# Performance work log

Hardware: AMD Instinct MI355X
Metric: run time of the kernel (lower is better)

## Reference

```python
import jax, jax.numpy as jnp
import numpy as np
from jax import lax

B, C, H, W = 16, 512, 32, 32
CQ = C // 8  # 64
EPS = 1e-5
NEG_SLOPE = 0.2


def _conv1x1(x, Wm, b):
    # x: [B,C,H,W], Wm: [O,C] (1x1 conv kernel squeezed), b: [O]
    return jnp.einsum('oc,bchw->bohw', Wm, x) + b[None, :, None, None]


def _calc_mean_std(feat):
    b, c = feat.shape[:2]
    v = feat.reshape(b, c, -1)
    mean = v.mean(axis=2)[:, :, None, None]
    var = v.var(axis=2, ddof=1) + EPS  # torch .var is unbiased
    std = jnp.sqrt(var)[:, :, None, None]
    return mean, std


def setup_inputs() -> dict:
    key = jax.random.key(0)
    ks = jax.random.split(key, 8)
    s = 0.02
    return {
        'inp': jax.random.normal(ks[0], (B, C, H, W), jnp.float32),
        'x': jax.random.normal(ks[1], (B, C, H, W), jnp.float32),
        'y': jax.random.normal(ks[2], (B, C, H, W), jnp.float32),
        'Wq': jax.random.normal(ks[3], (CQ, C), jnp.float32) * s,
        'bq': jnp.zeros((CQ,), jnp.float32),
        'Wk': jax.random.normal(ks[4], (CQ, C), jnp.float32) * s,
        'bk': jnp.zeros((CQ,), jnp.float32),
        'Wv': jax.random.normal(ks[5], (C, C), jnp.float32) * s,
        'bv': jnp.zeros((C,), jnp.float32),
        'Wc': jax.random.normal(ks[6], (C, 2 * C, 3, 3), jnp.float32) * s,
        'bc': jnp.zeros((C,), jnp.float32),
        'alpha': jnp.ones((1,), jnp.float32),
        'beta': jnp.ones((1,), jnp.float32),
    }


def reference(inp, x, y, Wq, bq, Wk, bk, Wv, bv, Wc, bc, alpha, beta):
    b, c, h, w = x.shape
    n = h * w
    t = float(CQ) ** 0.5  # default temperature sqrt(c_in//8)

    # --- identity-row attention: query from x, key from y ---
    pq = _conv1x1(x, Wq, bq).reshape(b, CQ, n)   # [b,cq,n]
    pk = _conv1x1(y, Wk, bk).reshape(b, CQ, n)
    pv = _conv1x1(x, Wv, bv).reshape(b, c, n)    # [b,c,n]
    attn_iden = jax.nn.softmax(jnp.einsum('bcn,bcm->bnm', pq, pk) / t, axis=-1)

    # --- pose-row attention: query from y, key from x ---
    pq_p = _conv1x1(y, Wq, bq).reshape(b, CQ, n)
    pk_p = _conv1x1(x, Wk, bk).reshape(b, CQ, n)
    attn_pose = jax.nn.softmax(jnp.einsum('bcn,bcm->bnm', pq_p, pk_p) / t, axis=-1)

    # x_update = bmm(value, attn_iden^T): out[c,m] = sum_n pv[c,n]*attn[m,n]
    x_update = jnp.einsum('bcn,bmn->bcm', pv, attn_iden).reshape(b, c, h, w)
    x_update = (1.0 - beta) * x + beta * x_update

    # --- AdaIN: normalize inp, re-affine with x stats ---
    t_mean, t_std = _calc_mean_std(x)
    i_mean, i_std = _calc_mean_std(inp)
    adained = (inp - i_mean) / i_std * t_std + t_mean

    # reverse attention combine with (1 - attn_pose)
    rev = jnp.einsum('bcn,bmn->bcm', adained.reshape(b, c, n), 1.0 - attn_pose)
    rev = rev.reshape(b, c, h, w)
    rev = (1.0 - alpha) * rev + alpha * adained

    # --- conv_comp: 3x3 conv (2C -> C), same padding, LeakyReLU(0.2) ---
    cat = jnp.concatenate([x_update, rev], axis=1)  # [b,2c,h,w]
    out = lax.conv_general_dilated(
        cat, Wc, window_strides=(1, 1), padding='SAME',
        dimension_numbers=('NCHW', 'OIHW', 'NCHW'))
    out = out + bc[None, :, None, None]
    out = jnp.where(out >= 0, out, NEG_SLOPE * out)
    return out
```

## Files before the change

kernel.cpp:

```cpp
#include <hip/hip_runtime.h>

typedef unsigned short u16;
typedef unsigned int u32;

using bf16x8 = __attribute__((ext_vector_type(8))) __bf16;
using f32x4  = __attribute__((ext_vector_type(4))) float;
using u16x4  = __attribute__((ext_vector_type(4))) unsigned short;

__device__ __forceinline__ f32x4 MFMA(bf16x8 a, bf16x8 b, f32x4 c) {
    return __builtin_amdgcn_mfma_f32_16x16x32_bf16(a, b, c, 0, 0, 0);
}

__device__ __forceinline__ u16 f2bf(float f) {
    u32 u = __builtin_bit_cast(u32, f);
    u = (u + 0x7FFFu + ((u >> 16) & 1u)) >> 16;
    return (u16)u;
}
__device__ __forceinline__ float bf2f(u16 h) {
    return __builtin_bit_cast(float, (u32)h << 16);
}

typedef const __attribute__((address_space(1))) unsigned int* gp_t;
typedef __attribute__((address_space(3))) unsigned int* lp_t;

__device__ __forceinline__ void gload16(const void* g, void* l) {
    __builtin_amdgcn_global_load_lds((gp_t)g, (lp_t)l, 16, 0, 0);
}

#define NPADR  1156

static constexpr size_t OFF_XT   = 0;
static constexpr size_t OFF_YT   = OFF_XT  + (size_t)16*1024*512*2;
static constexpr size_t OFF_PJX  = OFF_YT  + (size_t)16*1024*512*2;
static constexpr size_t OFF_PJY  = OFF_PJX + (size_t)16*1024*128*2;
static constexpr size_t OFF_PV   = OFF_PJY + (size_t)16*1024*128*2;
static constexpr size_t OFF_AD   = OFF_PV  + (size_t)16*512*1024*2;
static constexpr size_t OFF_ATTN = OFF_AD  + (size_t)16*512*1024*2;
static constexpr size_t OFF_ATT2 = OFF_ATTN+ (size_t)16*1024*1024*2;
static constexpr size_t OFF_CATT = OFF_ATT2+ (size_t)16*1024*1024*2;
static constexpr size_t OFF_WQK  = OFF_CATT+ (size_t)16*1156*1024*2;
static constexpr size_t OFF_WV   = OFF_WQK + (size_t)128*512*2;
static constexpr size_t OFF_WT   = OFF_WV  + (size_t)512*512*2;
static constexpr size_t OFF_SA   = OFF_WT  + (size_t)9*512*1024*2;
static constexpr size_t OFF_OA   = OFF_SA  + (size_t)16*512*4;
static constexpr size_t OFF_TM   = OFF_OA  + (size_t)16*512*4;

__global__ __launch_bounds__(256) void k_prep_w(const float* __restrict__ Wq,
                                                const float* __restrict__ Wk,
                                                const float* __restrict__ Wv,
                                                u16* __restrict__ wqk, u16* __restrict__ wv) {
    int i = blockIdx.x * 256 + threadIdx.x;
    if (i < 128 * 512) {
        float v = (i < 64 * 512) ? Wq[i] : Wk[i - 64 * 512];
        wqk[i] = f2bf(v);
    }
    if (i < 512 * 512) wv[i] = f2bf(Wv[i]);
}

__global__ __launch_bounds__(256) void k_prep_wt(const float* __restrict__ Wc, u16* __restrict__ wt) {
    int e = blockIdx.x * 256 + threadIdx.x;
    const float* src = Wc + (size_t)e * 9;
#pragma unroll
    for (int tap = 0; tap < 9; tap++) wt[(size_t)tap * 524288 + e] = f2bf(src[tap]);
}

__global__ __launch_bounds__(256) void k_border(u16* __restrict__ catT) {
    int cell = blockIdx.x, b = blockIdx.y;
    int row, col;
    if (cell < 34)       { row = 0;  col = cell; }
    else if (cell < 68)  { row = 33; col = cell - 34; }
    else if (cell < 100) { row = cell - 68 + 1;  col = 0; }
    else                 { row = cell - 100 + 1; col = 33; }
    u16* dst = catT + ((size_t)b * NPADR + row * 34 + col) * 1024;
    u16x4 z = {0, 0, 0, 0};
    ((u16x4*)dst)[threadIdx.x] = z;
}

__global__ __launch_bounds__(256) void k_stats(const float* __restrict__ x, const float* __restrict__ inp,
                                               u16* __restrict__ ad, float* __restrict__ tmA) {
    int row = blockIdx.x;
    int t = threadIdx.x;
    const float4* xr = (const float4*)(x + (size_t)row * 1024);
    const float4* ir = (const float4*)(inp + (size_t)row * 1024);
    float4 a = xr[t], c = ir[t];
    float s1 = a.x + a.y + a.z + a.w;
    float s2 = a.x * a.x + a.y * a.y + a.z * a.z + a.w * a.w;
    float p1 = c.x + c.y + c.z + c.w;
    float p2 = c.x * c.x + c.y * c.y + c.z * c.z + c.w * c.w;
#pragma unroll
    for (int m = 32; m; m >>= 1) {
        s1 += __shfl_xor(s1, m); s2 += __shfl_xor(s2, m);
        p1 += __shfl_xor(p1, m); p2 += __shfl_xor(p2, m);
    }
    __shared__ float red[4][4];
    __shared__ float bcast[2];
    int wv = t >> 6;
    if ((t & 63) == 0) { red[wv][0] = s1; red[wv][1] = s2; red[wv][2] = p1; red[wv][3] = p2; }
    __syncthreads();
    if (t == 0) {
        s1 = red[0][0] + red[1][0] + red[2][0] + red[3][0];
        s2 = red[0][1] + red[1][1] + red[2][1] + red[3][1];
        p1 = red[0][2] + red[1][2] + red[2][2] + red[3][2];
        p2 = red[0][3] + red[1][3] + red[2][3] + red[3][3];
        float tm = s1 * (1.0f / 1024.0f);
        float ts = sqrtf((s2 - 1024.0f * tm * tm) * (1.0f / 1023.0f) + 1e-5f);
        float im = p1 * (1.0f / 1024.0f);
        float is = sqrtf((p2 - 1024.0f * im * im) * (1.0f / 1023.0f) + 1e-5f);
        float sc = ts / is;
        bcast[0] = sc; bcast[1] = tm - im * sc;
        tmA[row] = tm;
    }
    __syncthreads();
    float sc = bcast[0], of = bcast[1];
    u16x4 r;
    r[0] = f2bf(c.x * sc + of); r[1] = f2bf(c.y * sc + of);
    r[2] = f2bf(c.z * sc + of); r[3] = f2bf(c.w * sc + of);
    ((u16x4*)(ad + (size_t)row * 1024))[t] = r;
}

__global__ __launch_bounds__(256) void k_transpose(const float* __restrict__ x, const float* __restrict__ y,
                                                   u16* __restrict__ xT, u16* __restrict__ yT) {
    __shared__ float tile[64][65];
    int b = blockIdx.y;
    int ct = blockIdx.x >> 4;
    int nt = blockIdx.x & 15;
    const float* src = blockIdx.z ? y : x;
    u16* dst = blockIdx.z ? yT : xT;
    int c0 = ct * 64, n0 = nt * 64;
    int ln = threadIdx.x & 63, wv = threadIdx.x >> 6;
#pragma unroll
    for (int i = 0; i < 16; i++) {
        int cl = wv + i * 4;
        tile[cl][ln] = src[((size_t)(b * 512 + c0 + cl)) * 1024 + n0 + ln];
    }
    __syncthreads();
#pragma unroll
    for (int i = 0; i < 16; i++) {
        int nl = wv + i * 4;
        dst[((size_t)(b * 1024 + n0 + nl)) * 512 + c0 + ln] = f2bf(tile[ln][nl]);
    }
}

template <int KTOT, int LDA, int LDB>
__device__ __forceinline__ void gemm128(const u16* __restrict__ Aorig, const u16* __restrict__ Borig,
                                        f32x4 (&acc)[4][4]) {
    __shared__ __align__(16) u16 lds[32768];
    constexpr int NT = KTOT / 32;
    const int tid = threadIdx.x;
    const int l = tid & 63, w = tid >> 6;
    const int lr = l & 15, lg = l >> 4;
    const int moff = (w >> 1) * 64, coff = (w & 1) * 64;
    char* ldsb = (char*)lds;
    auto stage = [&](const u16* orig, int ldx, int bufByte) {
#pragma unroll
        for (int it = 0; it < 2; it++) {
            int slot = it * 256 + tid;
            gload16(orig + (size_t)(slot & 127) * ldx + (slot >> 7) * 8,
                    ldsb + bufByte + it * 4096 + w * 1024);
        }
    };
    auto stageT = [&](int t, int s) {
        stage(Aorig + t * 32, LDA, s * 8192);
        stage(Borig + t * 32, LDB, 32768 + s * 8192);
    };
    stageT(0, 0);
    stageT(1, 1);
    stageT(2, 2);
#pragma unroll 1
    for (int q = 0; q < NT; q++) {
        int qq = q + 3; if (qq >= NT) qq -= NT;
        stageT(qq, (q + 3) & 3);
        asm volatile("s_waitcnt vmcnt(12)" ::: "memory");
        __builtin_amdgcn_s_barrier();
        const char* A = ldsb + (q & 3) * 8192;
        const char* B = ldsb + 32768 + (q & 3) * 8192;
        bf16x8 af[4], bb[4];
#pragma unroll
        for (int i = 0; i < 4; i++) af[i] = *(const bf16x8*)(A + lg * 2048 + (moff + 16 * i + lr) * 16);
#pragma unroll
        for (int i = 0; i < 4; i++) bb[i] = *(const bf16x8*)(B + lg * 2048 + (coff + 16 * i + lr) * 16);
        __builtin_amdgcn_s_setprio(1);
#pragma unroll
        for (int ri = 0; ri < 4; ri++)
#pragma unroll
            for (int ci = 0; ci < 4; ci++) acc[ri][ci] = MFMA(af[ri], bb[ci], acc[ri][ci]);
        __builtin_amdgcn_s_setprio(0);
        __builtin_amdgcn_s_barrier();
    }
    asm volatile("s_waitcnt vmcnt(0)" ::: "memory");
}

__global__ __launch_bounds__(256) void k_proj(const u16* __restrict__ xT, const u16* __restrict__ yT,
                                              const u16* __restrict__ wqk, const float* __restrict__ bq,
                                              const float* __restrict__ bk, u16* __restrict__ pjx,
                                              u16* __restrict__ pjy) {
    int b = blockIdx.y;
    const u16* S = blockIdx.z ? yT : xT;
    u16* D = blockIdx.z ? pjy : pjx;
    int nb = blockIdx.x * 128;
    f32x4 acc[4][4];
#pragma unroll
    for (int i = 0; i < 4; i++)
#pragma unroll
        for (int j = 0; j < 4; j++) acc[i][j] = f32x4{0.f, 0.f, 0.f, 0.f};
    gemm128<512, 512, 512>(S + ((size_t)b * 1024 + nb) * 512, wqk, acc);
    int l = threadIdx.x & 63, w = threadIdx.x >> 6;
    int lr = l & 15, lg = l >> 4;
    int moff = (w >> 1) * 64, coff = (w & 1) * 64;
#pragma unroll
    for (int ri = 0; ri < 4; ri++) {
#pragma unroll
        for (int r = 0; r < 4; r++) {
            int n = nb + moff + 16 * ri + 4 * lg + r;
#pragma unroll
            for (int ci = 0; ci < 4; ci++) {
                int cq = coff + 16 * ci + lr;
                float bias = (cq < 64) ? bq[cq] : bk[cq - 64];
                D[((size_t)b * 1024 + n) * 128 + cq] = f2bf(acc[ri][ci][r] + bias);
            }
        }
    }
}

__global__ __launch_bounds__(256) void k_pv(const u16* __restrict__ xT, const u16* __restrict__ wv,
                                            const float* __restrict__ bv, u16* __restrict__ pv) {
    int b = blockIdx.z;
    int mb = blockIdx.y * 128;
    int nb = blockIdx.x * 128;
    f32x4 acc[4][4];
#pragma unroll
    for (int i = 0; i < 4; i++)
#pragma unroll
        for (int j = 0; j < 4; j++) acc[i][j] = f32x4{0.f, 0.f, 0.f, 0.f};
    gemm128<512, 512, 512>(wv + (size_t)mb * 512, xT + ((size_t)b * 1024 + nb) * 512, acc);
    int l = threadIdx.x & 63, w = threadIdx.x >> 6;
    int lr = l & 15, lg = l >> 4;
    int moff = (w >> 1) * 64, coff = (w & 1) * 64;
#pragma unroll
    for (int ri = 0; ri < 4; ri++) {
#pragma unroll
        for (int r = 0; r < 4; r++) {
            int co = mb + moff + 16 * ri + 4 * lg + r;
            float bias = bv[co];
#pragma unroll
            for (int ci = 0; ci < 4; ci++) {
                int n = nb + coff + 16 * ci + lr;
                pv[((size_t)b * 512 + co) * 1024 + n] = f2bf(acc[ri][ci][r] + bias);
            }
        }
    }
}

__global__ __launch_bounds__(256) void k_score(const u16* __restrict__ pjx, const u16* __restrict__ pjy,
                                               u16* __restrict__ attnA, u16* __restrict__ attnB) {
    const u16* qT = blockIdx.y ? pjy : pjx;
    const u16* kT = blockIdx.y ? pjx : pjy;
    u16* attn = blockIdx.y ? attnB : attnA;
    int g = blockIdx.x * 4 + (threadIdx.x >> 6);
    int b = g >> 6, rb = g & 63;
    int l = threadIdx.x & 63, lr = l & 15, lg = l >> 4;
    int mb = rb * 16;
    const u16* qbase = qT + ((size_t)b * 1024 + mb + lr) * 128 + lg * 8;
    bf16x8 a0 = *(const bf16x8*)(qbase);
    bf16x8 a1 = *(const bf16x8*)(qbase + 32);
    const u16* kbase = kT + ((size_t)b * 1024 + lr) * 128 + 64 + lg * 8;
    f32x4 zero = {0.f, 0.f, 0.f, 0.f};
    float mrun[4] = {-1e30f, -1e30f, -1e30f, -1e30f};
    float srun[4] = {0.f, 0.f, 0.f, 0.f};
    for (int cf = 0; cf < 64; cf++) {
        bf16x8 b0 = *(const bf16x8*)(kbase + (size_t)cf * 16 * 128);
        bf16x8 b1 = *(const bf16x8*)(kbase + (size_t)cf * 16 * 128 + 32);
        f32x4 acc = zero;
        acc = MFMA(a0, b0, acc);
        acc = MFMA(a1, b1, acc);
#pragma unroll
        for (int r = 0; r < 4; r++) {
            float v = acc[r] * 0.125f;
            float mn = fmaxf(mrun[r], v);
            srun[r] = srun[r] * __expf(mrun[r] - mn) + __expf(v - mn);
            mrun[r] = mn;
        }
    }
#pragma unroll
    for (int m = 1; m < 16; m <<= 1) {
#pragma unroll
        for (int r = 0; r < 4; r++) {
            float mo = __shfl_xor(mrun[r], m);
            float so = __shfl_xor(srun[r], m);
            float mn = fmaxf(mrun[r], mo);
            srun[r] = srun[r] * __expf(mrun[r] - mn) + so * __expf(mo - mn);
            mrun[r] = mn;
        }
    }
    float inv[4];
#pragma unroll
    for (int r = 0; r < 4; r++) inv[r] = 1.0f / srun[r];
    for (int cf = 0; cf < 64; cf++) {
        bf16x8 b0 = *(const bf16x8*)(kbase + (size_t)cf * 16 * 128);
        bf16x8 b1 = *(const bf16x8*)(kbase + (size_t)cf * 16 * 128 + 32);
        f32x4 acc = zero;
        acc = MFMA(a0, b0, acc);
        acc = MFMA(a1, b1, acc);
#pragma unroll
        for (int r = 0; r < 4; r++) {
            float v = __expf(acc[r] * 0.125f - mrun[r]) * inv[r];
            attn[((size_t)b * 1024 + mb + 4 * lg + r) * 1024 + cf * 16 + lr] = f2bf(v);
        }
    }
}

__global__ __launch_bounds__(256) void k_value(const u16* __restrict__ attnA, const u16* __restrict__ attnB,
                                               const u16* __restrict__ pv, const u16* __restrict__ ad,
                                               const u16* __restrict__ xT, const float* __restrict__ tmA,
                                               const float* __restrict__ alpha, const float* __restrict__ beta,
                                               u16* __restrict__ catT) {
    int z = blockIdx.z;
    int b = z & 15, var = z >> 4;
    const u16* attn = var ? attnB : attnA;
    const u16* V = var ? ad : pv;
    int mb = blockIdx.x * 128;
    int cb = blockIdx.y * 128;
    f32x4 acc[4][4];
#pragma unroll
    for (int i = 0; i < 4; i++)
#pragma unroll
        for (int j = 0; j < 4; j++) acc[i][j] = f32x4{0.f, 0.f, 0.f, 0.f};
    gemm128<1024, 1024, 1024>(attn + ((size_t)b * 1024 + mb) * 1024,
                              V + ((size_t)b * 512 + cb) * 1024, acc);
    int l = threadIdx.x & 63, w = threadIdx.x >> 6;
    int lr = l & 15, lg = l >> 4;
    int moff = (w >> 1) * 64, coff = (w & 1) * 64;
    float sc = var ? alpha[0] : beta[0];
#pragma unroll
    for (int ri = 0; ri < 4; ri++) {
#pragma unroll
        for (int r = 0; r < 4; r++) {
            int m = mb + moff + 16 * ri + 4 * lg + r;
            int pidx = ((m >> 5) + 1) * 34 + (m & 31) + 1;
#pragma unroll
            for (int ci = 0; ci < 4; ci++) {
                int c = cb + coff + 16 * ci + lr;
                float av = acc[ri][ci][r];
                float res;
                if (var == 0) {
                    float xv = bf2f(xT[((size_t)b * 1024 + m) * 512 + c]);
                    res = (1.f - sc) * xv + sc * av;
                } else {
                    float tm = tmA[b * 512 + c];
                    float adv = bf2f(ad[((size_t)b * 512 + c) * 1024 + m]);
                    res = (1.f - sc) * (1024.f * tm - av) + sc * adv;
                }
                catT[((size_t)b * NPADR + pidx) * 1024 + (var ? 512 : 0) + c] = f2bf(res);
            }
        }
    }
}

__global__ __launch_bounds__(256, 2) void k_conv(const u16* __restrict__ wt, const u16* __restrict__ catT,
                                                 const float* __restrict__ bc, float* __restrict__ out) {
    extern __shared__ __align__(16) char dyn[];
    const int tid = threadIdx.x;
    const int l = tid & 63, w = tid >> 6;
    const int lr = l & 15, lg = l >> 4;
    const int b = blockIdx.z;
    const int ob = blockIdx.x * 128;
    const int pb = blockIdx.y * 128;
    const int r0 = blockIdx.y * 4;
    const int ooff = (w >> 1) * 64, poff = (w & 1) * 64;
    const u16* catB = catT + (size_t)b * NPADR * 1024 + (size_t)r0 * 34 * 1024;

    auto stageB = [&](int ckb, int bsel) {
        char* base = dyn + 40960 + bsel * 16384;
        const u16* src0 = catB + ckb;
#pragma unroll
        for (int it = 0; it < 4; it++) {
            if (tid < 204)
                gload16(src0 + (size_t)tid * 1024 + it * 8, base + it * 4096 + w * 1024);
        }
    };
    auto stageA = [&](int tap, int ckb, int slot) {
        char* base = dyn + slot * 8192;
        const u16* src0 = wt + ((size_t)tap * 512 + ob) * 1024 + ckb;
#pragma unroll
        for (int it = 0; it < 2; it++) {
            int s = it * 256 + tid;
            gload16(src0 + (size_t)(s & 127) * 1024 + (s >> 7) * 8,
                    base + it * 4096 + w * 1024);
        }
    };

    int aoff[4], rbase[4];
#pragma unroll
    for (int i = 0; i < 4; i++) {
        aoff[i] = lg * 2048 + (ooff + 16 * i + lr) * 16;
        int p = poff + 16 * i + lr;
        rbase[i] = ((p >> 5) + 1) * 34 + (p & 31) + 1;
    }

    f32x4 acc[4][4];
#pragma unroll
    for (int i = 0; i < 4; i++)
#pragma unroll
        for (int j = 0; j < 4; j++) acc[i][j] = f32x4{0.f, 0.f, 0.f, 0.f};

    stageA(0, 0, 0);
    stageB(0, 0);
    stageA(1, 0, 1);
    stageA(2, 0, 2);
    stageA(3, 0, 3);
    int phase = 0;
#pragma unroll 1
    for (int ckI = 0; ckI < 32; ckI++) {
#pragma unroll
        for (int tap = 0; tap < 9; tap++, phase++) {
            {
                int t4 = tap + 4;
                int c4 = ckI + (t4 >= 9);
                if (t4 >= 9) t4 -= 9;
                if (c4 >= 32) c4 = 0;
                stageA(t4, c4 * 32, (phase + 4) % 5);
            }
            if (tap == 5) {
                int cn = ckI + 1;
                stageB((cn >= 32 ? 0 : cn) * 32, cn & 1);
            }
            if (tap >= 5) asm volatile("s_waitcnt vmcnt(12)" ::: "memory");
            else          asm volatile("s_waitcnt vmcnt(8)" ::: "memory");
            __builtin_amdgcn_s_barrier();
            const char* A = dyn + (phase % 5) * 8192;
            const char* B = dyn + 40960 + (ckI & 1) * 16384;
            const int drow = (tap / 3 - 1) * 34 + (tap % 3 - 1);
            bf16x8 af[4], bb[4];
#pragma unroll
            for (int i = 0; i < 4; i++) af[i] = *(const bf16x8*)(A + aoff[i]);
#pragma unroll
            for (int i = 0; i < 4; i++) bb[i] = *(const bf16x8*)(B + lg * 4096 + (rbase[i] + drow) * 16);
            __builtin_amdgcn_s_setprio(1);
#pragma unroll
            for (int ri = 0; ri < 4; ri++)
#pragma unroll
                for (int ci = 0; ci < 4; ci++) acc[ri][ci] = MFMA(af[ri], bb[ci], acc[ri][ci]);
            __builtin_amdgcn_s_setprio(0);
            __builtin_amdgcn_s_barrier();
        }
    }
    asm volatile("s_waitcnt vmcnt(0)" ::: "memory");
#pragma unroll
    for (int ri = 0; ri < 4; ri++) {
#pragma unroll
        for (int r = 0; r < 4; r++) {
            int o = ob + ooff + 16 * ri + 4 * lg + r;
            float bias = bc[o];
#pragma unroll
            for (int ci = 0; ci < 4; ci++) {
                int p = pb + poff + 16 * ci + lr;
                float v = acc[ri][ci][r] + bias;
                v = (v >= 0.f) ? v : 0.2f * v;
                out[((size_t)b * 512 + o) * 1024 + p] = v;
            }
        }
    }
}

extern "C" void kernel_launch(void* const* d_in, const int* in_sizes, int n_in,
                              void* d_out, int out_size, void* d_ws, size_t ws_size,
                              hipStream_t stream) {
    (void)in_sizes; (void)n_in; (void)out_size; (void)ws_size;
    const float* inp = (const float*)d_in[0];
    const float* x   = (const float*)d_in[1];
    const float* y   = (const float*)d_in[2];
    const float* Wq  = (const float*)d_in[3];
    const float* bq  = (const float*)d_in[4];
    const float* Wk  = (const float*)d_in[5];
    const float* bk  = (const float*)d_in[6];
    const float* Wv  = (const float*)d_in[7];
    const float* bv  = (const float*)d_in[8];
    const float* Wc  = (const float*)d_in[9];
    const float* bc  = (const float*)d_in[10];
    const float* alpha = (const float*)d_in[11];
    const float* beta  = (const float*)d_in[12];
    float* out = (float*)d_out;

    char* ws = (char*)d_ws;
    u16* xT   = (u16*)(ws + OFF_XT);
    u16* yT   = (u16*)(ws + OFF_YT);
    u16* pjx  = (u16*)(ws + OFF_PJX);
    u16* pjy  = (u16*)(ws + OFF_PJY);
    u16* pv   = (u16*)(ws + OFF_PV);
    u16* ad   = (u16*)(ws + OFF_AD);
    u16* attnA = (u16*)(ws + OFF_ATTN);
    u16* attnB = (u16*)(ws + OFF_ATT2);
    u16* catT = (u16*)(ws + OFF_CATT);
    u16* wqk  = (u16*)(ws + OFF_WQK);
    u16* wv   = (u16*)(ws + OFF_WV);
    u16* wt   = (u16*)(ws + OFF_WT);
    float* tmA = (float*)(ws + OFF_TM);

    hipFuncSetAttribute((const void*)k_conv, hipFuncAttributeMaxDynamicSharedMemorySize, 73728);

    k_prep_w<<<1024, 256, 0, stream>>>(Wq, Wk, Wv, wqk, wv);
    k_prep_wt<<<2048, 256, 0, stream>>>(Wc, wt);
    k_border<<<dim3(132, 16), 256, 0, stream>>>(catT);
    k_stats<<<8192, 256, 0, stream>>>(x, inp, ad, tmA);
    k_transpose<<<dim3(128, 16, 2), 256, 0, stream>>>(x, y, xT, yT);
    k_proj<<<dim3(8, 16, 2), 256, 0, stream>>>(xT, yT, wqk, bq, bk, pjx, pjy);
    k_pv<<<dim3(8, 4, 16), 256, 0, stream>>>(xT, wv, bv, pv);
    k_score<<<dim3(256, 2), 256, 0, stream>>>(pjx, pjy, attnA, attnB);
    k_value<<<dim3(8, 4, 32), 256, 0, stream>>>(attnA, attnB, pv, ad, xT, tmA, alpha, beta, catT);
    k_conv<<<dim3(4, 8, 16), 256, 73728, stream>>>(wt, catT, bc, out);
}
```

Baseline: 439.9 us.

## Enlarge conv tile to 256 pixels with 8-wave blocks and shallower weight pipeline

The implicit-GEMM 3x3 conv now uses 512-thread blocks covering 128 output channels by 256 pixels (8 image rows), halving the number of blocks along the pixel axis. Each weight tile staged in LDS is therefore reused by twice as many pixels, and the halo overhead per input tile drops (10 padded rows for 8 output rows instead of 6 for 4). To fit LDS, the weight ring buffer shrinks from 5 to 3 slots, so prefetch runs 2 taps ahead instead of 4. This lowers global traffic per FLOP but risks more exposed load latency and lower occupancy with 512-thread blocks.

```diff
diff --git a/kernel.cpp b/kernel.cpp
--- a/kernel.cpp
+++ b/kernel.cpp
@@ -356,7 +356,7 @@
     }
 }
 
-__global__ __launch_bounds__(256, 2) void k_conv(const u16* __restrict__ wt, const u16* __restrict__ catT,
+__global__ __launch_bounds__(512, 2) void k_conv(const u16* __restrict__ wt, const u16* __restrict__ catT,
                                                  const float* __restrict__ bc, float* __restrict__ out) {
     extern __shared__ __align__(16) char dyn[];
     const int tid = threadIdx.x;
@@ -364,36 +364,34 @@
     const int lr = l & 15, lg = l >> 4;
     const int b = blockIdx.z;
     const int ob = blockIdx.x * 128;
-    const int pb = blockIdx.y * 128;
-    const int r0 = blockIdx.y * 4;
-    const int ooff = (w >> 1) * 64, poff = (w & 1) * 64;
+    const int pb = blockIdx.y * 256;
+    const int r0 = blockIdx.y * 8;
+    const int ow = w >> 2, pw = w & 3;
     const u16* catB = catT + (size_t)b * NPADR * 1024 + (size_t)r0 * 34 * 1024;
 
-    auto stageB = [&](int ckb, int bsel) {
-        char* base = dyn + 40960 + bsel * 16384;
-        const u16* src0 = catB + ckb;
-#pragma unroll
-        for (int it = 0; it < 4; it++) {
-            if (tid < 204)
-                gload16(src0 + (size_t)tid * 1024 + it * 8, base + it * 4096 + w * 1024);
-        }
+    auto stageA = [&](int tap, int ck, int slot) {
+        char* base = dyn + slot * 8192;
+        int row = tid & 127, g = tid >> 7;
+        gload16(wt + ((size_t)tap * 512 + ob + row) * 1024 + ck + g * 8,
+                base + g * 2048 + row * 16);
     };
-    auto stageA = [&](int tap, int ckb, int slot) {
-        char* base = dyn + slot * 8192;
-        const u16* src0 = wt + ((size_t)tap * 512 + ob) * 1024 + ckb;
-#pragma unroll
-        for (int it = 0; it < 2; it++) {
-            int s = it * 256 + tid;
-            gload16(src0 + (size_t)(s & 127) * 1024 + (s >> 7) * 8,
-                    base + it * 4096 + w * 1024);
+    auto stageB = [&](int ck, int sel) {
+        char* base = dyn + 24576 + sel * 24576;
+#pragma unroll
+        for (int it = 0; it < 3; it++) {
+            int idx = it * 512 + tid;
+            int g = idx / 384;
+            int row = idx - g * 384;
+            gload16(catB + (size_t)row * 1024 + ck + g * 8,
+                    base + g * 6144 + row * 16);
         }
     };
 
     int aoff[4], rbase[4];
 #pragma unroll
     for (int i = 0; i < 4; i++) {
-        aoff[i] = lg * 2048 + (ooff + 16 * i + lr) * 16;
-        int p = poff + 16 * i + lr;
+        aoff[i] = lg * 2048 + (ow * 64 + 16 * i + lr) * 16;
+        int p = pw * 64 + 16 * i + lr;
         rbase[i] = ((p >> 5) + 1) * 34 + (p & 31) + 1;
     }
 
@@ -406,35 +404,33 @@
     stageA(0, 0, 0);
     stageB(0, 0);
     stageA(1, 0, 1);
-    stageA(2, 0, 2);
-    stageA(3, 0, 3);
     int phase = 0;
 #pragma unroll 1
     for (int ckI = 0; ckI < 32; ckI++) {
 #pragma unroll
         for (int tap = 0; tap < 9; tap++, phase++) {
             {
-                int t4 = tap + 4;
-                int c4 = ckI + (t4 >= 9);
-                if (t4 >= 9) t4 -= 9;
-                if (c4 >= 32) c4 = 0;
-                stageA(t4, c4 * 32, (phase + 4) % 5);
+                int t2 = tap + 2;
+                int c2 = ckI + (t2 >= 9);
+                if (t2 >= 9) t2 -= 9;
+                if (c2 >= 32) c2 = 0;
+                stageA(t2, c2 * 32, (phase + 2) % 3);
             }
             if (tap == 5) {
                 int cn = ckI + 1;
                 stageB((cn >= 32 ? 0 : cn) * 32, cn & 1);
             }
-            if (tap >= 5) asm volatile("s_waitcnt vmcnt(12)" ::: "memory");
-            else          asm volatile("s_waitcnt vmcnt(8)" ::: "memory");
+            if (tap >= 5 && tap <= 7) asm volatile("s_waitcnt vmcnt(5)" ::: "memory");
+            else                      asm volatile("s_waitcnt vmcnt(2)" ::: "memory");
             __builtin_amdgcn_s_barrier();
-            const char* A = dyn + (phase % 5) * 8192;
-            const char* B = dyn + 40960 + (ckI & 1) * 16384;
+            const char* A = dyn + (phase % 3) * 8192;
+            const char* B = dyn + 24576 + (ckI & 1) * 24576;
             const int drow = (tap / 3 - 1) * 34 + (tap % 3 - 1);
             bf16x8 af[4], bb[4];
 #pragma unroll
             for (int i = 0; i < 4; i++) af[i] = *(const bf16x8*)(A + aoff[i]);
 #pragma unroll
-            for (int i = 0; i < 4; i++) bb[i] = *(const bf16x8*)(B + lg * 4096 + (rbase[i] + drow) * 16);
+            for (int i = 0; i < 4; i++) bb[i] = *(const bf16x8*)(B + lg * 6144 + (rbase[i] + drow) * 16);
             __builtin_amdgcn_s_setprio(1);
 #pragma unroll
             for (int ri = 0; ri < 4; ri++)
@@ -449,11 +445,11 @@
     for (int ri = 0; ri < 4; ri++) {
 #pragma unroll
         for (int r = 0; r < 4; r++) {
-            int o = ob + ooff + 16 * ri + 4 * lg + r;
+            int o = ob + ow * 64 + 16 * ri + 4 * lg + r;
             float bias = bc[o];
 #pragma unroll
             for (int ci = 0; ci < 4; ci++) {
-                int p = pb + poff + 16 * ci + lr;
+                int p = pb + pw * 64 + 16 * ci + lr;
                 float v = acc[ri][ci][r] + bias;
                 v = (v >= 0.f) ? v : 0.2f * v;
                 out[((size_t)b * 512 + o) * 1024 + p] = v;
@@ -507,5 +503,5 @@
     k_pv<<<dim3(8, 4, 16), 256, 0, stream>>>(xT, wv, bv, pv);
     k_score<<<dim3(256, 2), 256, 0, stream>>>(pjx, pjy, attnA, attnB);
     k_value<<<dim3(8, 4, 32), 256, 0, stream>>>(attnA, attnB, pv, ad, xT, tmA, alpha, beta, catT);
-    k_conv<<<dim3(4, 8, 16), 256, 73728, stream>>>(wt, catT, bc, out);
-}
+    k_conv<<<dim3(4, 4, 16), 512, 73728, stream>>>(wt, catT, bc, out);
+}
```

Measured after the change: 406.6 us. 7.6% less time.
